# Kernel tuning notes

Hardware: AMD Instinct MI355X
Metric: run time of the kernel (lower is better)

Reference implementation:

```python
import jax, jax.numpy as jnp
import numpy as np

B, S, DIM, H, DH, FF = 2, 2048, 2048, 16, 128, 8192
EPS = 1e-6


def rmsnorm(x, g):
    xf = x.astype(jnp.float32)
    y = xf * jax.lax.rsqrt(jnp.mean(xf * xf, axis=-1, keepdims=True) + EPS)
    return y.astype(x.dtype) * g


def rope_cache(seq_len, head_dim):
    inv_freq = 1.0 / (10000.0 ** (jnp.arange(0, head_dim, 2, dtype=jnp.float32) / head_dim))
    t = jnp.arange(seq_len, dtype=jnp.float32)
    freqs = jnp.outer(t, inv_freq)              # [S, DH/2]
    emb = jnp.concatenate([freqs, freqs], -1)   # [S, DH]
    return jnp.cos(emb), jnp.sin(emb)


def rotate_half(x):
    x1, x2 = jnp.split(x, 2, axis=-1)
    return jnp.concatenate([-x2, x1], axis=-1)


def apply_rope(x, cos, sin):
    # x: [B,H,S,DH]; cos/sin: [S,DH] broadcast per position
    c = cos[None, None, :, :]
    s = sin[None, None, :, :]
    return x * c + rotate_half(x) * s


def setup_inputs() -> dict:
    key = jax.random.key(0)
    ks = jax.random.split(key, 10)
    std = 0.02
    x = jax.random.normal(ks[0], (B, S, DIM), jnp.float32)
    mask = jnp.tril(jnp.ones((S, S), dtype=bool))[None, None]  # causal [1,1,S,S]
    wq = jax.random.normal(ks[1], (H * DH, DIM), jnp.float32) * std
    wk = jax.random.normal(ks[2], (H * DH, DIM), jnp.float32) * std
    wv = jax.random.normal(ks[3], (H * DH, DIM), jnp.float32) * std
    wo = jax.random.normal(ks[4], (DIM, H * DH), jnp.float32) * std
    w1 = jax.random.normal(ks[5], (FF, DIM), jnp.float32) * std
    w2 = jax.random.normal(ks[6], (DIM, FF), jnp.float32) * std
    w3 = jax.random.normal(ks[7], (FF, DIM), jnp.float32) * std
    g_attn = jnp.ones((DIM,), jnp.float32)
    g_ffn = jnp.ones((DIM,), jnp.float32)
    return {"x": x, "mask": mask, "wq": wq, "wk": wk, "wv": wv, "wo": wo,
            "w1": w1, "w2": w2, "w3": w3, "g_attn": g_attn, "g_ffn": g_ffn}


def reference(x, mask, wq, wk, wv, wo, w1, w2, w3, g_attn, g_ffn):
    b, s, _ = x.shape
    scale = 1.0 / np.sqrt(DH)
    # --- attention sublayer ---
    h = rmsnorm(x, g_attn)
    q = jnp.einsum('bsd,ed->bse', h, wq).reshape(b, s, H, DH).transpose(0, 2, 1, 3)
    k = jnp.einsum('bsd,ed->bse', h, wk).reshape(b, s, H, DH).transpose(0, 2, 1, 3)
    v = jnp.einsum('bsd,ed->bse', h, wv).reshape(b, s, H, DH).transpose(0, 2, 1, 3)
    cos, sin = rope_cache(s, DH)
    q = apply_rope(q, cos, sin)
    k = apply_rope(k, cos, sin)
    scores = jnp.einsum('bhqd,bhkd->bhqk', q, k) * scale
    scores = jnp.where(mask, scores, -1e9)
    attn = jax.nn.softmax(scores, axis=-1)
    o = jnp.einsum('bhqk,bhkd->bhqd', attn, v)
    o = o.transpose(0, 2, 1, 3).reshape(b, s, H * DH)
    x = x + jnp.einsum('bse,de->bsd', o, wo)
    # --- SwiGLU FFN sublayer ---
    h2 = rmsnorm(x, g_ffn)
    u = jnp.einsum('bsd,fd->bsf', h2, w1)
    g = jnp.einsum('bsd,fd->bsf', h2, w3)
    ff = jnp.einsum('bsf,df->bsd', jax.nn.silu(u) * g, w2)
    return x + ff
```

## Files before the change

### kernel.cpp

```cpp
#include <hip/hip_runtime.h>
#include <hip/hip_bf16.h>
#include <math.h>

typedef __hip_bfloat16 bf16;
typedef short short8 __attribute__((ext_vector_type(8)));
typedef float f32x4 __attribute__((ext_vector_type(4)));

#define Bq 2
#define Sq 2048
#define Dq 2048
#define Hq 16
#define DHq 128
#define FFq 8192
#define Mq 4096


__device__ __forceinline__ float b2f(bf16 x) { return __bfloat162float(x); }
__device__ __forceinline__ bf16 f2b(float x) { return __float2bfloat16(x); }

__device__ __forceinline__ void gload16(const void* g, void* lds_base) {
  __builtin_amdgcn_global_load_lds(
      (const __attribute__((address_space(1))) void*)g,
      (__attribute__((address_space(3))) void*)lds_base,
      16, 0, 0);
}

__global__ __launch_bounds__(256)
void conv_k(const float* __restrict__ src, bf16* __restrict__ dst, long n) {
  const long stride = (long)gridDim.x * 256 * 8;
  for (long i = ((long)blockIdx.x * 256 + threadIdx.x) * 8; i < n; i += stride) {
    f32x4 a = *(const f32x4*)(src + i);
    f32x4 b = *(const f32x4*)(src + i + 4);
    union { short8 s; bf16 h[8]; } u;
#pragma unroll
    for (int j = 0; j < 4; ++j) { u.h[j] = f2b(a[j]); u.h[j + 4] = f2b(b[j]); }
    *(short8*)(dst + i) = u.s;
  }
}

template <int EPI>
__global__ __launch_bounds__(256)
void gemm3(const bf16* __restrict__ A, const bf16* __restrict__ Bt,
           const void* __restrict__ R, void* __restrict__ C,
           int N, int K, int ldb, long long boff) {
  __shared__ __align__(16) bf16 As[128][64];
  __shared__ __align__(16) bf16 Bs[128][64];
  const int tid = threadIdx.x;
  const int w = tid >> 6;
  const int l = tid & 63;

  const int nwg = gridDim.x * gridDim.y;
  const int orig = blockIdx.x + blockIdx.y * gridDim.x;
  const int qq = nwg >> 3, rr8 = nwg & 7;
  const int xcd = orig & 7, idx8 = orig >> 3;
  const int wg = (xcd < rr8 ? xcd * (qq + 1) : rr8 * (qq + 1) + (xcd - rr8) * qq) + idx8;
  const int bm = (wg / gridDim.x) * 128;
  const int bn = (wg % gridDim.x) * 128;

  const int wr = (w >> 1) * 64;
  const int wc = (w & 1) * 64;
  f32x4 acc[4][4] = {};

  const bf16* Ab = A + (size_t)bm * K;
  const bf16* Bb = Bt + (size_t)bn * ldb + (size_t)boff;

  const int sRow = w * 8 + (l >> 3);
  const int sCol = (((l & 7) ^ (l >> 3)) << 3);

  for (int kt = 0; kt < K; kt += 64) {
    __syncthreads();
#pragma unroll
    for (int i = 0; i < 4; ++i) {
      gload16(Ab + (size_t)(i * 32 + sRow) * K + kt + sCol, &As[i * 32 + w * 8][0]);
      gload16(Bb + (size_t)(i * 32 + sRow) * ldb + kt + sCol, &Bs[i * 32 + w * 8][0]);
    }
    __syncthreads();

#pragma unroll
    for (int kk = 0; kk < 2; ++kk) {
      short8 af[4], bfv[4];
#pragma unroll
      for (int m = 0; m < 4; ++m) {
        const int ra = wr + m * 16 + (l & 15);
        af[m] = *(const short8*)&As[ra][(((kk * 4 + (l >> 4)) ^ (ra & 7)) << 3)];
      }
#pragma unroll
      for (int n = 0; n < 4; ++n) {
        const int rb = wc + n * 16 + (l & 15);
        bfv[n] = *(const short8*)&Bs[rb][(((kk * 4 + (l >> 4)) ^ (rb & 7)) << 3)];
      }
#pragma unroll
      for (int m = 0; m < 4; ++m)
#pragma unroll
        for (int n = 0; n < 4; ++n)
          acc[m][n] = __builtin_amdgcn_mfma_f32_16x16x32_bf16(af[m], bfv[n], acc[m][n], 0, 0, 0);
    }
  }

  const int rbase = bm + wr + (l >> 4) * 4;
  const int cbase = bn + wc + (l & 15);
#pragma unroll
  for (int m = 0; m < 4; ++m)
#pragma unroll
    for (int r = 0; r < 4; ++r) {
      const int row = rbase + m * 16 + r;
#pragma unroll
      for (int n = 0; n < 4; ++n) {
        const size_t idx = (size_t)row * N + (cbase + n * 16);
        float vacc = acc[m][n][r];
        if (EPI == 1) {
          ((float*)C)[idx] = vacc + ((const float*)R)[idx];
        } else if (EPI == 2) {
          const float u = b2f(((const bf16*)R)[idx]);
          ((bf16*)C)[idx] = f2b((u / (1.f + expf(-u))) * vacc);
        } else {
          ((bf16*)C)[idx] = f2b(vacc);
        }
      }
    }
}

template <int EPI>
__global__ __launch_bounds__(256)
void gemm2(const bf16* __restrict__ A, const float* __restrict__ Bt,
           const void* __restrict__ R, void* __restrict__ C,
           int N, int K, int ldb, long long boff) {
  __shared__ __align__(16) bf16 As[128][64];
  __shared__ __align__(16) float Bsf[128][64];
  const int tid = threadIdx.x;
  const int w = tid >> 6;
  const int l = tid & 63;

  const int nwg = gridDim.x * gridDim.y;
  const int orig = blockIdx.x + blockIdx.y * gridDim.x;
  const int qq = nwg >> 3, rr8 = nwg & 7;
  const int xcd = orig & 7, idx8 = orig >> 3;
  const int wg = (xcd < rr8 ? xcd * (qq + 1) : rr8 * (qq + 1) + (xcd - rr8) * qq) + idx8;
  const int bm = (wg / gridDim.x) * 128;
  const int bn = (wg % gridDim.x) * 128;

  const int wr = (w >> 1) * 64;
  const int wc = (w & 1) * 64;
  f32x4 acc[4][4] = {};

  const bf16* Ab = A + (size_t)bm * K;
  const float* Bb = Bt + (size_t)bn * ldb + (size_t)boff;

  const int aSrcCol = (((l & 7) ^ (l >> 3)) << 3);
  const int bKey = (w * 4 + (l >> 4)) & 7;
  const int bSrcCol = (((l & 15) ^ bKey) << 2);

  for (int kt = 0; kt < K; kt += 64) {
    __syncthreads();
#pragma unroll
    for (int i = 0; i < 4; ++i)
      gload16(Ab + (size_t)(i * 32 + w * 8 + (l >> 3)) * K + kt + aSrcCol,
              &As[i * 32 + w * 8][0]);
#pragma unroll
    for (int i = 0; i < 8; ++i)
      gload16(Bb + (size_t)(i * 16 + w * 4 + (l >> 4)) * ldb + kt + bSrcCol,
              &Bsf[i * 16 + w * 4][0]);
    __syncthreads();

#pragma unroll
    for (int kk = 0; kk < 2; ++kk) {
      short8 af[4], bfv[4];
#pragma unroll
      for (int m = 0; m < 4; ++m) {
        const int ra = wr + m * 16 + (l & 15);
        const int pb = (kk * 4 + (l >> 4)) ^ (ra & 7);
        af[m] = *(const short8*)&As[ra][pb * 8];
      }
#pragma unroll
      for (int n = 0; n < 4; ++n) {
        const int rb = wc + n * 16 + (l & 15);
        const int b0 = kk * 8 + (l >> 4) * 2;
        const f32x4 x0 = *(const f32x4*)&Bsf[rb][(b0 ^ (rb & 7)) * 4];
        const f32x4 x1 = *(const f32x4*)&Bsf[rb][((b0 + 1) ^ (rb & 7)) * 4];
        union { short8 s; bf16 h[8]; } u;
#pragma unroll
        for (int j = 0; j < 4; ++j) { u.h[j] = f2b(x0[j]); u.h[j + 4] = f2b(x1[j]); }
        bfv[n] = u.s;
      }
#pragma unroll
      for (int m = 0; m < 4; ++m)
#pragma unroll
        for (int n = 0; n < 4; ++n)
          acc[m][n] = __builtin_amdgcn_mfma_f32_16x16x32_bf16(af[m], bfv[n], acc[m][n], 0, 0, 0);
    }
  }

  const int rbase = bm + wr + (l >> 4) * 4;
  const int cbase = bn + wc + (l & 15);
#pragma unroll
  for (int m = 0; m < 4; ++m)
#pragma unroll
    for (int r = 0; r < 4; ++r) {
      const int row = rbase + m * 16 + r;
#pragma unroll
      for (int n = 0; n < 4; ++n) {
        const size_t idx = (size_t)row * N + (cbase + n * 16);
        float vacc = acc[m][n][r];
        if (EPI == 1) {
          ((float*)C)[idx] = vacc + ((const float*)R)[idx];
        } else if (EPI == 2) {
          const float u = b2f(((const bf16*)R)[idx]);
          ((bf16*)C)[idx] = f2b((u / (1.f + expf(-u))) * vacc);
        } else {
          ((bf16*)C)[idx] = f2b(vacc);
        }
      }
    }
}

__global__ __launch_bounds__(256)
void rmsnorm_k(const float* __restrict__ xin, const float* __restrict__ g,
               bf16* __restrict__ out) {
  const int row = blockIdx.x;
  const int tid = threadIdx.x;
  const float* xp = xin + (size_t)row * Dq + tid * 8;
  f32x4 a = *(const f32x4*)xp, b = *(const f32x4*)(xp + 4);
  float xf[8];
#pragma unroll
  for (int j = 0; j < 4; ++j) { xf[j] = a[j]; xf[j + 4] = b[j]; }
  float ss = 0.f;
#pragma unroll
  for (int j = 0; j < 8; ++j) ss += xf[j] * xf[j];
#pragma unroll
  for (int off = 32; off > 0; off >>= 1) ss += __shfl_down(ss, off);
  __shared__ float red[4];
  if ((tid & 63) == 0) red[tid >> 6] = ss;
  __syncthreads();
  const float rms = rsqrtf((red[0] + red[1] + red[2] + red[3]) * (1.f / (float)Dq) + 1e-6f);
  const float* gp = g + tid * 8;
  f32x4 ga = *(const f32x4*)gp, gb = *(const f32x4*)(gp + 4);
  union { short8 s; bf16 h[8]; } uo;
#pragma unroll
  for (int j = 0; j < 4; ++j) {
    uo.h[j] = f2b(xf[j] * rms * ga[j]);
    uo.h[j + 4] = f2b(xf[j + 4] * rms * gb[j]);
  }
  *(short8*)(out + (size_t)row * Dq + tid * 8) = uo.s;
}

__global__ __launch_bounds__(256)
void rope_k(bf16* __restrict__ q, bf16* __restrict__ k, int ld) {
  const size_t idx = (size_t)blockIdx.x * 256 + threadIdx.x;
  const int i = (int)(idx & 63);
  const int h = (int)((idx >> 6) & 15);
  const int s = (int)((idx >> 10) & 2047);
  const int b = (int)(idx >> 21);
  const float f = (float)s * powf(10000.f, -(float)i * (1.f / 64.f));
  float sn, cs;
  sincosf(f, &sn, &cs);
  const size_t base = ((size_t)(b * Sq + s)) * ld + h * DHq + i;
  const float qa = b2f(q[base]), qb_ = b2f(q[base + 64]);
  q[base] = f2b(qa * cs - qb_ * sn);
  q[base + 64] = f2b(qb_ * cs + qa * sn);
  const float ka = b2f(k[base]), kb_ = b2f(k[base + 64]);
  k[base] = f2b(ka * cs - kb_ * sn);
  k[base + 64] = f2b(kb_ * cs + ka * sn);
}

__device__ __forceinline__ int swz8(int row) { return (((row >> 3) ^ row) & 7) << 3; }

#define ATTN_COMPUTE(AQ, QB, QROW, M_, L_, OACC, KV0, CUR)                        \
  {                                                                               \
    f32x4 sc[4] = {};                                                             \
    __builtin_amdgcn_s_setprio(1);                                                \
    _Pragma("unroll") for (int n = 0; n < 4; ++n) {                               \
      const int krow = n * 16 + c;                                                \
      const int sw = swz8(krow);                                                  \
      _Pragma("unroll") for (int kk = 0; kk < 4; ++kk) {                          \
        short8 ak = *(const short8*)&Ks[CUR][krow][(kk * 32 + g * 8) ^ sw];       \
        sc[n] = __builtin_amdgcn_mfma_f32_16x16x32_bf16(ak, AQ[kk], sc[n], 0, 0, 0); \
      }                                                                           \
    }                                                                             \
    __builtin_amdgcn_s_setprio(0);                                                \
    float p[4][4];                                                                \
    float tmax = -3.0e38f;                                                        \
    if ((KV0) + 63 <= (QB)) {                                                     \
      _Pragma("unroll") for (int n = 0; n < 4; ++n)                               \
        _Pragma("unroll") for (int r = 0; r < 4; ++r) {                           \
          const float val = sc[n][r] * SCALE;                                     \
          p[n][r] = val;                                                          \
          tmax = fmaxf(tmax, val);                                                \
        }                                                                         \
    } else {                                                                      \
      _Pragma("unroll") for (int n = 0; n < 4; ++n)                               \
        _Pragma("unroll") for (int r = 0; r < 4; ++r) {                           \
          const int kvg = (KV0) + n * 16 + g * 4 + r;                             \
          float val = sc[n][r] * SCALE;                                           \
          if (kvg > (QROW)) val = -3.0e38f;                                       \
          p[n][r] = val;                                                          \
          tmax = fmaxf(tmax, val);                                                \
        }                                                                         \
    }                                                                             \
    tmax = fmaxf(tmax, __shfl_xor(tmax, 16));                                     \
    tmax = fmaxf(tmax, __shfl_xor(tmax, 32));                                     \
    const bool grow = !__all(tmax <= M_);                                         \
    const float m_new = grow ? fmaxf(M_, tmax) : M_;                              \
    float tsum = 0.f;                                                             \
    _Pragma("unroll") for (int n = 0; n < 4; ++n)                                 \
      _Pragma("unroll") for (int r = 0; r < 4; ++r) {                             \
        const float pv = expf(p[n][r] - m_new);                                   \
        p[n][r] = pv;                                                             \
        tsum += pv;                                                               \
      }                                                                           \
    tsum += __shfl_xor(tsum, 16);                                                 \
    tsum += __shfl_xor(tsum, 32);                                                 \
    if (grow) {                                                                   \
      const float corr = expf(M_ - m_new);                                        \
      L_ = L_ * corr + tsum;                                                      \
      M_ = m_new;                                                                 \
      _Pragma("unroll") for (int dt = 0; dt < 8; ++dt) OACC[dt] *= corr;          \
    } else {                                                                      \
      L_ += tsum;                                                                 \
    }                                                                             \
    const int keyc = (c ^ (c >> 3)) & 7;                                          \
    _Pragma("unroll") for (int n = 0; n < 4; ++n) {                               \
      union { unsigned long long u; bf16 hh[4]; } pk;                             \
      _Pragma("unroll") for (int r = 0; r < 4; ++r) pk.hh[r] = f2b(p[n][r]);      \
      const int blk = (2 * n + (g >> 1)) ^ keyc;                                  \
      *(unsigned long long*)&Ps[w][c][blk * 8 + (g & 1) * 4] = pk.u;              \
    }                                                                             \
    short8 ap[2];                                                                 \
    _Pragma("unroll") for (int kk = 0; kk < 2; ++kk)                              \
      ap[kk] = *(const short8*)&Ps[w][c][(kk * 32 + g * 8) ^ (keyc << 3)];        \
    __builtin_amdgcn_s_setprio(1);                                                \
    _Pragma("unroll") for (int dt = 0; dt < 8; ++dt) {                            \
      const int vrow = dt * 16 + c;                                               \
      const int vsw = swz8(vrow);                                                 \
      _Pragma("unroll") for (int kk = 0; kk < 2; ++kk) {                          \
        short8 av = *(const short8*)&Vt[CUR][vrow][(kk * 32 + g * 8) ^ vsw];      \
        OACC[dt] = __builtin_amdgcn_mfma_f32_16x16x32_bf16(av, ap[kk], OACC[dt], 0, 0, 0); \
      }                                                                           \
    }                                                                             \
    __builtin_amdgcn_s_setprio(0);                                                \
  }

__global__ __launch_bounds__(512)
void attn_k(const bf16* __restrict__ q, const bf16* __restrict__ k,
            const bf16* __restrict__ v, bf16* __restrict__ o, int ld) {
  __shared__ __align__(16) bf16 Ks[2][64][128];
  __shared__ __align__(16) bf16 Vt[2][128][64];
  __shared__ __align__(16) bf16 Ps[8][16][64];
  const int tid = threadIdx.x;
  const int w = tid >> 6, l = tid & 63;
  const int g = l >> 4, c = l & 15;
  const int x = blockIdx.x;
  const int h = blockIdx.y;
  const int b = blockIdx.z;
  const size_t hoff = (size_t)h * DHq;
  const float SCALE = 0.08838834764831845f;

  const int q0h = (15 - x) * 128, q0l = x * 128;
  const int qbh = q0h + w * 16, qbl = q0l + w * 16;
  const int qrh = qbh + c, qrl = qbl + c;

  short8 aqh[4], aql[4];
  {
    const bf16* qph = q + (size_t)(b * Sq + qrh) * ld + hoff + g * 8;
    const bf16* qpl = q + (size_t)(b * Sq + qrl) * ld + hoff + g * 8;
#pragma unroll
    for (int kk = 0; kk < 4; ++kk) {
      aqh[kk] = *(const short8*)(qph + kk * 32);
      aql[kk] = *(const short8*)(qpl + kk * 32);
    }
  }

  float mh = -3.0e38f, lh = 0.f, ml = -3.0e38f, ll_ = 0.f;
  f32x4 oh[8] = {}, ol[8] = {};

  const int stRow = tid >> 4;
  const int stBlk = tid & 15;
  const int ntiles = (q0h >> 6) + 2;

  {
#pragma unroll
    for (int i = 0; i < 2; ++i) {
      const int kr = i * 32 + w * 4 + (l >> 4);
      const int key = (kr ^ (kr >> 3)) & 7;
      gload16(k + (size_t)(b * Sq + kr) * ld + hoff + ((c ^ key) << 3),
              &Ks[0][i * 32 + w * 4][0]);
    }
    const int c0 = stBlk * 8;
#pragma unroll
    for (int i = 0; i < 2; ++i) {
      const int vr = i * 32 + stRow;
      union { short8 s; bf16 hh[8]; } uv;
      uv.s = *(const short8*)(v + (size_t)(b * Sq + vr) * ld + hoff + c0);
#pragma unroll
      for (int j = 0; j < 8; ++j) Vt[0][c0 + j][vr ^ swz8(c0 + j)] = uv.hh[j];
    }
  }
  __syncthreads();

  for (int t = 0; t < ntiles; ++t) {
    const int cur = t & 1, nxt = cur ^ 1;
    const int kv0 = t * 64;
    const bool pf = (t + 1 < ntiles);
    short8 vpa, vpb;
    if (pf) {
      const int kvn = kv0 + 64;
#pragma unroll
      for (int i = 0; i < 2; ++i) {
        const int kr = i * 32 + w * 4 + (l >> 4);
        const int key = (kr ^ (kr >> 3)) & 7;
        gload16(k + (size_t)(b * Sq + kvn + kr) * ld + hoff + ((c ^ key) << 3),
                &Ks[nxt][i * 32 + w * 4][0]);
      }
      vpa = *(const short8*)(v + (size_t)(b * Sq + kvn + stRow) * ld + hoff + stBlk * 8);
      vpb = *(const short8*)(v + (size_t)(b * Sq + kvn + 32 + stRow) * ld + hoff + stBlk * 8);
    }

    if (kv0 <= qbh + 15) ATTN_COMPUTE(aqh, qbh, qrh, mh, lh, oh, kv0, cur);

    if (pf) {
      const int c0 = stBlk * 8;
      union { short8 s; bf16 hh[8]; } uv;
      uv.s = vpa;
#pragma unroll
      for (int j = 0; j < 8; ++j) Vt[nxt][c0 + j][stRow ^ swz8(c0 + j)] = uv.hh[j];
      uv.s = vpb;
#pragma unroll
      for (int j = 0; j < 8; ++j) Vt[nxt][c0 + j][(32 + stRow) ^ swz8(c0 + j)] = uv.hh[j];
    }

    if (kv0 <= qbl + 15) ATTN_COMPUTE(aql, qbl, qrl, ml, ll_, ol, kv0, cur);

    __syncthreads();
  }

  {
    const float inv = 1.f / lh;
    bf16* op = o + (size_t)(b * Sq + qrh) * Dq + hoff + g * 4;
#pragma unroll
    for (int dt = 0; dt < 8; ++dt) {
      union { unsigned long long u; bf16 hh[4]; } pk;
#pragma unroll
      for (int r = 0; r < 4; ++r) pk.hh[r] = f2b(oh[dt][r] * inv);
      *(unsigned long long*)(op + dt * 16) = pk.u;
    }
  }
  {
    const float inv = 1.f / ll_;
    bf16* op = o + (size_t)(b * Sq + qrl) * Dq + hoff + g * 4;
#pragma unroll
    for (int dt = 0; dt < 8; ++dt) {
      union { unsigned long long u; bf16 hh[4]; } pk;
#pragma unroll
      for (int r = 0; r < 4; ++r) pk.hh[r] = f2b(ol[dt][r] * inv);
      *(unsigned long long*)(op + dt * 16) = pk.u;
    }
  }
}

extern "C" void kernel_launch(void* const* d_in, const int* in_sizes, int n_in,
                              void* d_out, int out_size, void* d_ws, size_t ws_size,
                              hipStream_t stream) {
  (void)in_sizes; (void)n_in; (void)out_size;
  const float* x  = (const float*)d_in[0];
  const float* wq = (const float*)d_in[2];
  const float* wk = (const float*)d_in[3];
  const float* wv = (const float*)d_in[4];
  const float* wo = (const float*)d_in[5];
  const float* w1 = (const float*)d_in[6];
  const float* w2 = (const float*)d_in[7];
  const float* w3 = (const float*)d_in[8];
  const float* ga = (const float*)d_in[9];
  const float* gf = (const float*)d_in[10];
  float* out = (float*)d_out;

  char* ws = (char*)d_ws;
  dim3 blk(256);
  dim3 gA(8, Hq, Bq);
  dim3 blkA(512);

  const size_t SZ_H   = (size_t)Mq * Dq * 2;
  const size_t SZ_QKV = (size_t)Mq * 3 * Dq * 2;
  const size_t SZ_W4  = (size_t)Dq * Dq * 2;
  const size_t SZ_W13 = (size_t)FFq * Dq * 2;
  const size_t ACT    = SZ_H + SZ_QKV;
  const size_t WTS    = 3 * SZ_W4 + SZ_W4 + 3 * SZ_W13;
  const size_t NEED   = ACT + WTS;

  if (ws_size >= NEED) {
    bf16* h    = (bf16*)(ws);
    bf16* qkv  = (bf16*)(ws + SZ_H);
    bf16* ob   = h;
    bf16* h2   = qkv;
    bf16* ub   = (bf16*)(ws + SZ_H + SZ_H);
    char* wb   = ws + ACT;
    bf16* wqkv_b = (bf16*)(wb);
    bf16* wo_b   = (bf16*)(wb + 3 * SZ_W4);
    bf16* w1_b   = (bf16*)(wb + 4 * SZ_W4);
    bf16* w3_b   = (bf16*)(wb + 4 * SZ_W4 + SZ_W13);
    bf16* w2_b   = (bf16*)(wb + 4 * SZ_W4 + 2 * SZ_W13);

    const long nW4 = (long)Dq * Dq, nW13 = (long)FFq * Dq;
    conv_k<<<1024, blk, 0, stream>>>(wq, wqkv_b, nW4);
    conv_k<<<1024, blk, 0, stream>>>(wk, wqkv_b + nW4, nW4);
    conv_k<<<1024, blk, 0, stream>>>(wv, wqkv_b + 2 * nW4, nW4);
    conv_k<<<1024, blk, 0, stream>>>(wo, wo_b, nW4);
    conv_k<<<2048, blk, 0, stream>>>(w1, w1_b, nW13);
    conv_k<<<2048, blk, 0, stream>>>(w3, w3_b, nW13);
    conv_k<<<2048, blk, 0, stream>>>(w2, w2_b, nW13);

    rmsnorm_k<<<Mq, blk, 0, stream>>>(x, ga, h);
    gemm3<0><<<dim3(48, 32), blk, 0, stream>>>(h, wqkv_b, nullptr, qkv, 6144, Dq, Dq, 0);
    rope_k<<<(Bq * Sq * Hq * 64) / 256, blk, 0, stream>>>(qkv, qkv + Dq, 3 * Dq);
    attn_k<<<gA, blkA, 0, stream>>>(qkv, qkv + Dq, qkv + 2 * Dq, ob, 3 * Dq);
    gemm3<1><<<dim3(16, 32), blk, 0, stream>>>(ob, wo_b, x, out, Dq, Dq, Dq, 0);
    rmsnorm_k<<<Mq, blk, 0, stream>>>(out, gf, h2);
    for (int hh = 0; hh < 2; ++hh) {
      bf16* w1h = w1_b + (size_t)hh * 4096 * Dq;
      bf16* w3h = w3_b + (size_t)hh * 4096 * Dq;
      gemm3<0><<<dim3(32, 32), blk, 0, stream>>>(h2, w1h, nullptr, ub, 4096, Dq, Dq, 0);
      gemm3<2><<<dim3(32, 32), blk, 0, stream>>>(h2, w3h, ub, ub, 4096, Dq, Dq, 0);
      gemm3<1><<<dim3(16, 32), blk, 0, stream>>>(ub, w2_b, out, out, Dq, 4096, FFq,
                                                 (long long)hh * 4096);
    }
  } else {
    const size_t MS = (size_t)Mq * Dq * 2;
    bf16* h  = (bf16*)(ws);
    bf16* kb = (bf16*)(ws + MS);
    bf16* vb = (bf16*)(ws + 2 * MS);
    bf16* qb = (bf16*)(ws + 3 * MS);
    bf16* ub = (bf16*)(ws);
    bf16* ob = h;
    bf16* h2 = qb;

    dim3 gD(Dq / 128, Mq / 128);
    dim3 gU(32, Mq / 128);

    rmsnorm_k<<<Mq, blk, 0, stream>>>(x, ga, h);
    gemm2<0><<<gD, blk, 0, stream>>>(h, wq, nullptr, qb, Dq, Dq, Dq, 0);
    gemm2<0><<<gD, blk, 0, stream>>>(h, wk, nullptr, kb, Dq, Dq, Dq, 0);
    gemm2<0><<<gD, blk, 0, stream>>>(h, wv, nullptr, vb, Dq, Dq, Dq, 0);
    rope_k<<<(Bq * Sq * Hq * 64) / 256, blk, 0, stream>>>(qb, kb, Dq);
    attn_k<<<gA, blkA, 0, stream>>>(qb, kb, vb, ob, Dq);
    gemm2<1><<<gD, blk, 0, stream>>>(ob, wo, x, out, Dq, Dq, Dq, 0);
    rmsnorm_k<<<Mq, blk, 0, stream>>>(out, gf, h2);
    for (int hh = 0; hh < 2; ++hh) {
      const long long bo13 = (long long)hh * 4096 * 2048;
      gemm2<0><<<gU, blk, 0, stream>>>(h2, w1, nullptr, ub, 4096, Dq, Dq, bo13);
      gemm2<2><<<gU, blk, 0, stream>>>(h2, w3, ub, ub, 4096, Dq, Dq, bo13);
      gemm2<1><<<gD, blk, 0, stream>>>(ub, w2, out, out, Dq, 4096, FFq,
                                       (long long)hh * 4096);
    }
  }
}
```

Measured before the change: 953.3 us.

## Add 256x256-tile 8-wave GEMM with double-buffered LDS and interleaved MFMA phases

Adds a new GEMM kernel that uses 256x256 output tiles, 512 threads (8 waves) and double-buffered LDS. Loads go straight to LDS with an XOR swizzle, and LDS reads, global prefetch and MFMA quarters are interleaved under explicit barriers, waitcnts and priority hints. It replaces the 128x128 GEMM for the QKV, output-projection and W1/W3 matmuls; the W2 matmul keeps the old kernel. Larger tiles raise data reuse per byte loaded, but the grids become small (128-384 blocks) and the many barriers could cut occupancy and overlap.

```diff
diff --git a/kernel.cpp b/kernel.cpp
--- a/kernel.cpp
+++ b/kernel.cpp
@@ -14,7 +14,6 @@
 #define FFq 8192
 #define Mq 4096
 
-
 __device__ __forceinline__ float b2f(bf16 x) { return __bfloat162float(x); }
 __device__ __forceinline__ bf16 f2b(float x) { return __float2bfloat16(x); }
 
@@ -36,6 +35,129 @@
     for (int j = 0; j < 4; ++j) { u.h[j] = f2b(a[j]); u.h[j + 4] = f2b(b[j]); }
     *(short8*)(dst + i) = u.s;
   }
+}
+
+#define SB8()  __builtin_amdgcn_sched_barrier(0)
+#define BAR8() { asm volatile("" ::: "memory"); __builtin_amdgcn_s_barrier(); asm volatile("" ::: "memory"); }
+#define VMC4() { asm volatile("s_waitcnt vmcnt(4)" ::: "memory"); SB8(); }
+#define LGK0() { asm volatile("s_waitcnt lgkmcnt(0)" ::: "memory"); SB8(); }
+
+#define STG8(Gp, ldX, rowOff, kt, XsBuf)                                        \
+  gload16(Gp + (size_t)((rowOff) + w8 + lr) * (size_t)(ldX) + (kt) + sCol,      \
+          &XsBuf[(rowOff) + w8][0]);                                            \
+  gload16(Gp + (size_t)((rowOff) + 64 + w8 + lr) * (size_t)(ldX) + (kt) + sCol, \
+          &XsBuf[(rowOff) + 64 + w8][0]);
+
+#define RD_A8(dst, XsBuf, mb)                                                   \
+  _Pragma("unroll") for (int mi = 0; mi < 4; ++mi) {                            \
+    const int ra = wmBase + ((mb) + mi) * 16 + c;                               \
+    _Pragma("unroll") for (int kk = 0; kk < 2; ++kk)                            \
+      dst[mi][kk] = *(const short8*)&XsBuf[ra][(((kk * 4 + g) ^ (ra & 7)) << 3)]; \
+  }
+
+#define RD_B8(dst, XsBuf, nb_)                                                  \
+  _Pragma("unroll") for (int ni = 0; ni < 2; ++ni) {                            \
+    const int rb = wnBase + ((nb_) + ni) * 16 + c;                              \
+    _Pragma("unroll") for (int kk = 0; kk < 2; ++kk)                            \
+      dst[ni][kk] = *(const short8*)&XsBuf[rb][(((kk * 4 + g) ^ (rb & 7)) << 3)]; \
+  }
+
+#define MFMA_Q8(afv, bfv, mb, nb_)                                              \
+  __builtin_amdgcn_s_setprio(1);                                                \
+  _Pragma("unroll") for (int mi = 0; mi < 4; ++mi)                              \
+    _Pragma("unroll") for (int ni = 0; ni < 2; ++ni)                            \
+      _Pragma("unroll") for (int kk = 0; kk < 2; ++kk)                          \
+        acc[(mb) + mi][(nb_) + ni] = __builtin_amdgcn_mfma_f32_16x16x32_bf16(   \
+            afv[mi][kk], bfv[ni][kk], acc[(mb) + mi][(nb_) + ni], 0, 0, 0);     \
+  __builtin_amdgcn_s_setprio(0);
+
+template <int EPI>
+__global__ __launch_bounds__(512, 2)
+void gemm8(const bf16* __restrict__ A, const bf16* __restrict__ Bt,
+           const void* __restrict__ R, void* __restrict__ C,
+           int N, int K, int ldb, long long boff) {
+  __shared__ __align__(16) bf16 As[2][256][64];
+  __shared__ __align__(16) bf16 Bs[2][256][64];
+  const int tid = threadIdx.x;
+  const int w = tid >> 6, l = tid & 63;
+  const int g = l >> 4, c = l & 15;
+  const int w8 = w * 8, lr = l >> 3;
+  const int sCol = (((l & 7) ^ lr) << 3);
+
+  const int nwg = gridDim.x * gridDim.y;
+  const int orig = blockIdx.x + blockIdx.y * gridDim.x;
+  const int qq = nwg >> 3, rr8 = nwg & 7;
+  const int xcd = orig & 7, idx8 = orig >> 3;
+  const int wg = (xcd < rr8 ? xcd * (qq + 1) : rr8 * (qq + 1) + (xcd - rr8) * qq) + idx8;
+  const int bm = (wg / gridDim.x) * 256;
+  const int bn = (wg % gridDim.x) * 256;
+
+  const int wmBase = (w >> 2) * 128;
+  const int wnBase = (w & 3) * 64;
+
+  const bf16* Ab = A + (size_t)bm * K;
+  const bf16* Bb = Bt + (size_t)bn * ldb + (size_t)boff;
+
+  f32x4 acc[8][4] = {};
+  const int nt = K >> 6;
+
+  STG8(Ab, K, 0, 0, As[0]); STG8(Ab, K, 128, 0, As[0]);
+  STG8(Bb, ldb, 0, 0, Bs[0]); STG8(Bb, ldb, 128, 0, Bs[0]);
+  STG8(Bb, ldb, 0, 64, Bs[1]);
+  STG8(Ab, K, 0, 64, As[1]);
+  VMC4(); BAR8();
+
+  short8 af[4][2], bf[2][2], af2[4][2], bf2[2][2];
+  for (int it = 0; it < (nt >> 1); ++it) {
+    const int t = it * 2;
+    const int kt1 = (t + 1) << 6;
+    const int kt2 = (t + 2 < nt ? t + 2 : nt - 1) << 6;
+    const int kt3 = (t + 3 < nt ? t + 3 : nt - 1) << 6;
+    RD_A8(af, As[0], 0); RD_B8(bf, Bs[0], 0);
+    STG8(Ab, K, 128, kt1, As[1]);
+    BAR8(); LGK0(); MFMA_Q8(af, bf, 0, 0); BAR8();
+    RD_B8(bf2, Bs[0], 2);
+    STG8(Bb, ldb, 128, kt1, Bs[1]);
+    BAR8(); LGK0(); MFMA_Q8(af, bf2, 0, 2); BAR8();
+    RD_A8(af2, As[0], 4);
+    STG8(Bb, ldb, 0, kt2, Bs[0]);
+    BAR8(); LGK0(); MFMA_Q8(af2, bf, 4, 0); BAR8();
+    STG8(Ab, K, 0, kt2, As[0]);
+    VMC4(); BAR8(); MFMA_Q8(af2, bf2, 4, 2); BAR8();
+    RD_A8(af, As[1], 0); RD_B8(bf, Bs[1], 0);
+    STG8(Ab, K, 128, kt2, As[0]);
+    BAR8(); LGK0(); MFMA_Q8(af, bf, 0, 0); BAR8();
+    RD_B8(bf2, Bs[1], 2);
+    STG8(Bb, ldb, 128, kt2, Bs[0]);
+    BAR8(); LGK0(); MFMA_Q8(af, bf2, 0, 2); BAR8();
+    RD_A8(af2, As[1], 4);
+    STG8(Bb, ldb, 0, kt3, Bs[1]);
+    BAR8(); LGK0(); MFMA_Q8(af2, bf, 4, 0); BAR8();
+    STG8(Ab, K, 0, kt3, As[1]);
+    VMC4(); BAR8(); MFMA_Q8(af2, bf2, 4, 2); BAR8();
+  }
+
+  const int rbase = bm + wmBase + g * 4;
+  const int cbase = bn + wnBase + c;
+#pragma unroll
+  for (int m = 0; m < 8; ++m)
+#pragma unroll
+    for (int r = 0; r < 4; ++r) {
+      const int row = rbase + m * 16 + r;
+#pragma unroll
+      for (int n = 0; n < 4; ++n) {
+        const size_t idx = (size_t)row * N + (cbase + n * 16);
+        float vacc = acc[m][n][r];
+        if (EPI == 1) {
+          ((float*)C)[idx] = vacc + ((const float*)R)[idx];
+        } else if (EPI == 2) {
+          const float u = b2f(((const bf16*)R)[idx]);
+          ((bf16*)C)[idx] = f2b((u / (1.f + expf(-u))) * vacc);
+        } else {
+          ((bf16*)C)[idx] = f2b(vacc);
+        }
+      }
+    }
 }
 
 template <int EPI>
@@ -476,6 +598,7 @@
   dim3 blk(256);
   dim3 gA(8, Hq, Bq);
   dim3 blkA(512);
+  dim3 blk8(512);
 
   const size_t SZ_H   = (size_t)Mq * Dq * 2;
   const size_t SZ_QKV = (size_t)Mq * 3 * Dq * 2;
@@ -508,16 +631,16 @@
     conv_k<<<2048, blk, 0, stream>>>(w2, w2_b, nW13);
 
     rmsnorm_k<<<Mq, blk, 0, stream>>>(x, ga, h);
-    gemm3<0><<<dim3(48, 32), blk, 0, stream>>>(h, wqkv_b, nullptr, qkv, 6144, Dq, Dq, 0);
+    gemm8<0><<<dim3(24, 16), blk8, 0, stream>>>(h, wqkv_b, nullptr, qkv, 6144, Dq, Dq, 0);
     rope_k<<<(Bq * Sq * Hq * 64) / 256, blk, 0, stream>>>(qkv, qkv + Dq, 3 * Dq);
     attn_k<<<gA, blkA, 0, stream>>>(qkv, qkv + Dq, qkv + 2 * Dq, ob, 3 * Dq);
-    gemm3<1><<<dim3(16, 32), blk, 0, stream>>>(ob, wo_b, x, out, Dq, Dq, Dq, 0);
+    gemm8<1><<<dim3(8, 16), blk8, 0, stream>>>(ob, wo_b, x, out, Dq, Dq, Dq, 0);
     rmsnorm_k<<<Mq, blk, 0, stream>>>(out, gf, h2);
     for (int hh = 0; hh < 2; ++hh) {
       bf16* w1h = w1_b + (size_t)hh * 4096 * Dq;
       bf16* w3h = w3_b + (size_t)hh * 4096 * Dq;
-      gemm3<0><<<dim3(32, 32), blk, 0, stream>>>(h2, w1h, nullptr, ub, 4096, Dq, Dq, 0);
-      gemm3<2><<<dim3(32, 32), blk, 0, stream>>>(h2, w3h, ub, ub, 4096, Dq, Dq, 0);
+      gemm8<0><<<dim3(16, 16), blk8, 0, stream>>>(h2, w1h, nullptr, ub, 4096, Dq, Dq, 0);
+      gemm8<2><<<dim3(16, 16), blk8, 0, stream>>>(h2, w3h, ub, ub, 4096, Dq, Dq, 0);
       gemm3<1><<<dim3(16, 32), blk, 0, stream>>>(ub, w2_b, out, out, Dq, 4096, FFq,
                                                  (long long)hh * 4096);
     }
```

New measurement: 930.6 us. 2.4% less time.
